# Kernel tuning notes

Hardware: AMD Instinct MI355X
Metric: run time of the kernel (lower is better)

## Reference

```python
import jax, jax.numpy as jnp
import numpy as np

BN_EPS = 1e-5
TN_EPS = 1e-4


def binarize(x):
    # Clipped straight-through binarization (Courbariaux BNN / Brevitas 1-bit):
    # forward = sign(x) in {-1,+1}, backward = hardtanh STE.
    xc = jnp.clip(x, -1.0, 1.0)
    return xc + jax.lax.stop_gradient(jnp.where(x >= 0, 1.0, -1.0).astype(x.dtype) - xc)


def setup_inputs() -> dict:
    key = jax.random.key(0)
    ks = jax.random.split(key, 20)
    B, D, H, C = 16384, 1024, 1024, 10
    inp = {"x": jax.random.uniform(ks[0], (B, D), dtype=jnp.float32)}
    dims = [(H, D), (H, H), (H, H), (C, H)]
    for i, (o, n) in enumerate(dims):
        inp[f"W{i+1}"] = jax.random.uniform(ks[1 + i], (o, n), minval=-1.0, maxval=1.0, dtype=jnp.float32)
    # BatchNorm1d params (eval mode, running stats) for the 3 hidden layers
    for i in range(3):
        k0, k1, k2, k3 = jax.random.split(ks[5 + i], 4)
        inp[f"g{i+1}"] = 1.0 + 0.1 * jax.random.normal(k0, (H,), dtype=jnp.float32)
        inp[f"b{i+1}"] = 0.1 * jax.random.normal(k1, (H,), dtype=jnp.float32)
        inp[f"m{i+1}"] = 0.1 * jax.random.normal(k2, (H,), dtype=jnp.float32)
        inp[f"v{i+1}"] = 0.5 + jax.random.uniform(k3, (H,), dtype=jnp.float32)
    # TensorNorm (scalar norm on the logits)
    inp["tn_w"] = jnp.ones((), dtype=jnp.float32)
    inp["tn_b"] = jnp.zeros((), dtype=jnp.float32)
    inp["tn_m"] = jnp.zeros((), dtype=jnp.float32)
    inp["tn_v"] = jnp.ones((), dtype=jnp.float32)
    return inp


def reference(x, W1, W2, W3, W4,
              g1, b1, m1, v1,
              g2, b2, m2, v2,
              g3, b3, m3, v3,
              tn_w, tn_b, tn_m, tn_v):
    h = binarize(2.0 * x.reshape(x.shape[0], -1) - 1.0)
    # Dropout is identity in eval mode.
    bn = [(g1, b1, m1, v1), (g2, b2, m2, v2), (g3, b3, m3, v3)]
    for W, (g, b, m, v) in zip((W1, W2, W3), bn):
        h = h @ binarize(W).T                      # [B,H] fake-quant linear, no bias
        h = (h - m) * (g * jax.lax.rsqrt(v + BN_EPS)) + b  # BatchNorm1d eval
        h = binarize(h)                            # 1-bit activation quant
    h = h @ binarize(W4).T                         # [B,10]
    # TensorNorm: scalar affine normalization over the whole tensor
    return (h - tn_m) * jax.lax.rsqrt(tn_v + TN_EPS) * tn_w + tn_b
```

## Files before the change

kernel.cpp:

```cpp
#include <hip/hip_runtime.h>
#include <stdint.h>

typedef int  v4i  __attribute__((ext_vector_type(4)));
typedef int  v16i __attribute__((ext_vector_type(16)));
typedef unsigned int uint32;

#define BATCH 16384
#define FEAT  1024

#define OFF_ACTA 0u
#define OFF_ACTB 16777216u
#define OFF_WA1  33554432u
#define OFF_WA2  34603008u
#define OFF_WA3  35651584u
#define OFF_WA4  36700160u
#define OFF_TH   36732928u

__global__ void __launch_bounds__(256) prep_kernel(
    const float* __restrict__ x,
    const float* __restrict__ W1, const float* __restrict__ W2,
    const float* __restrict__ W3, const float* __restrict__ W4,
    const float* __restrict__ g1, const float* __restrict__ b1,
    const float* __restrict__ m1, const float* __restrict__ v1,
    const float* __restrict__ g2, const float* __restrict__ b2,
    const float* __restrict__ m2, const float* __restrict__ v2,
    const float* __restrict__ g3, const float* __restrict__ b3,
    const float* __restrict__ m3, const float* __restrict__ v3,
    char* __restrict__ actA, char* __restrict__ wa1, char* __restrict__ wa2,
    char* __restrict__ wa3, char* __restrict__ wa4, int2* __restrict__ TH)
{
    int b = blockIdx.x;
    if (b == 609) {
        for (int gid = threadIdx.x; gid < 3072; gid += 256) {
            int l = gid >> 10, j = gid & 1023;
            const float *g, *bb, *m, *v;
            if (l == 0)      { g = g1; bb = b1; m = m1; v = v1; }
            else if (l == 1) { g = g2; bb = b2; m = m2; v = v2; }
            else             { g = g3; bb = b3; m = m3; v = v3; }
            double gd = (double)g[j], bd = (double)bb[j], md = (double)m[j], vd = (double)v[j];
            double s = gd / sqrt(vd + 1e-5);
            int ti, flip;
            if (s > 0.0)      { ti = (int)ceil(md - bd / s);  flip = 0; }
            else if (s < 0.0) { ti = (int)floor(md - bd / s); flip = 1; }
            else              { ti = (bd >= 0.0) ? -2000000 : 2000000; flip = 0; }
            TH[gid] = make_int2(ti, flip);
        }
        return;
    }

    const float* src; char* dst; float thr; int nrows; int dblk;
    if (b < 512)      { src = x  + (size_t)b * 32768;            dst = actA; dblk = b;      thr = 0.5f; nrows = 32; }
    else if (b < 544) { int mb = b - 512; src = W1 + (size_t)mb * 32768; dst = wa1; dblk = mb; thr = 0.0f; nrows = 32; }
    else if (b < 576) { int mb = b - 544; src = W2 + (size_t)mb * 32768; dst = wa2; dblk = mb; thr = 0.0f; nrows = 32; }
    else if (b < 608) { int mb = b - 576; src = W3 + (size_t)mb * 32768; dst = wa3; dblk = mb; thr = 0.0f; nrows = 32; }
    else              { src = W4; dst = wa4; dblk = 0; thr = 0.0f; nrows = 10; }

    __shared__ unsigned char T[32][1040];
#pragma unroll
    for (int u = 0; u < 8; ++u) {
        int unit = threadIdx.x + u * 256;
        int row  = unit >> 6;
        int c16  = (unit & 63) << 4;
        uint32 wb0 = 0, wb1 = 0, wb2 = 0, wb3 = 0;
        if (row < nrows) {
            const float* p = src + (size_t)row * 1024 + c16;
            float4 f0 = *(const float4*)(p + 0);
            float4 f1 = *(const float4*)(p + 4);
            float4 f2 = *(const float4*)(p + 8);
            float4 f3 = *(const float4*)(p + 12);
            wb0 = (f0.x>=thr?0x01u:0xFFu) | ((f0.y>=thr?0x01u:0xFFu)<<8) | ((f0.z>=thr?0x01u:0xFFu)<<16) | ((f0.w>=thr?0x01u:0xFFu)<<24);
            wb1 = (f1.x>=thr?0x01u:0xFFu) | ((f1.y>=thr?0x01u:0xFFu)<<8) | ((f1.z>=thr?0x01u:0xFFu)<<16) | ((f1.w>=thr?0x01u:0xFFu)<<24);
            wb2 = (f2.x>=thr?0x01u:0xFFu) | ((f2.y>=thr?0x01u:0xFFu)<<8) | ((f2.z>=thr?0x01u:0xFFu)<<16) | ((f2.w>=thr?0x01u:0xFFu)<<24);
            wb3 = (f3.x>=thr?0x01u:0xFFu) | ((f3.y>=thr?0x01u:0xFFu)<<8) | ((f3.z>=thr?0x01u:0xFFu)<<16) | ((f3.w>=thr?0x01u:0xFFu)<<24);
        }
        *(uint4*)&T[row][c16] = make_uint4(wb0, wb1, wb2, wb3);
    }
    __syncthreads();

    int lane = threadIdx.x & 63;
    int wv   = threadIdx.x >> 6;
    int row  = lane & 31;
    int hb   = (lane >> 5) * 4;
#pragma unroll
    for (int u = 0; u < 8; ++u) {
        int kk = wv * 8 + u;
        const unsigned char* tr = &T[row][kk * 32 + hb];
        uint32 w0 = *(const uint32*)(tr + 0);
        uint32 w1 = *(const uint32*)(tr + 8);
        uint32 w2 = *(const uint32*)(tr + 16);
        uint32 w3 = *(const uint32*)(tr + 24);
        *(uint4*)(dst + (((size_t)dblk * 32 + kk) * 64 + lane) * 16) = make_uint4(w0, w1, w2, w3);
    }
}

__global__ void __launch_bounds__(256, 2) gemm_i8_kernel(
    const v4i* __restrict__ Af, const v4i* __restrict__ Bin,
    const int2* __restrict__ th, v4i* __restrict__ Bout)
{
    __shared__ v4i Bs[2][2048];
    const int tid  = threadIdx.x;
    const int lane = tid & 63;
    const int wv   = tid >> 6;
    int bid = blockIdx.x;
    int xcd = bid & 7;
    int i   = bid >> 3;
    int s   = xcd + ((i >> 3) << 3);
    int m   = i & 7;
    int mt  = m * 4 + wv;
    int nb0 = s * 8;

    v4i r[8];
    {
        const v4i* srcp = Bin + (size_t)nb0 * 2048;
#pragma unroll
        for (int j = 0; j < 8; ++j) r[j] = srcp[j * 256 + tid];
    }
    v4i a[32];
    {
        const v4i* Ap = Af + (size_t)mt * 2048;
#pragma unroll
        for (int kk = 0; kk < 32; ++kk) a[kk] = Ap[kk * 64 + lane];
    }
    int tt[16], tf[16];
    {
        const int2* thp = th + mt * 32;
        int hi4 = (lane >> 5) * 4;
#pragma unroll
        for (int q = 0; q < 16; ++q) {
            int2 t = thp[(q & 3) + 8 * (q >> 2) + hi4];
            tt[q] = t.x; tf[q] = t.y;
        }
    }
#pragma unroll
    for (int j = 0; j < 8; ++j) Bs[0][j * 256 + tid] = r[j];
    __syncthreads();

    int buf = 0;
#pragma unroll 1
    for (int it = 0; it < 8; ++it) {
        if (it < 7) {
            const v4i* srcp = Bin + (size_t)(nb0 + it + 1) * 2048;
#pragma unroll
            for (int j = 0; j < 8; ++j) r[j] = srcp[j * 256 + tid];
        }
        v16i acc;
#pragma unroll
        for (int z = 0; z < 16; ++z) acc[z] = 0;
#pragma unroll
        for (int kk = 0; kk < 32; ++kk) {
            v4i bfrag = Bs[buf][kk * 64 + lane];
            acc = __builtin_amdgcn_mfma_i32_32x32x32_i8(a[kk], bfrag, acc, 0, 0, 0);
        }
        uint32 wds0 = 0, wds1 = 0, wds2 = 0, wds3 = 0;
#pragma unroll
        for (int bq = 0; bq < 4; ++bq) {
            { int q = bq;      int h = acc[q]; int bit = tf[q] ? (h <= tt[q]) : (h >= tt[q]); wds0 |= (bit ? 0x01u : 0xFFu) << (8 * bq); }
            { int q = 4 + bq;  int h = acc[q]; int bit = tf[q] ? (h <= tt[q]) : (h >= tt[q]); wds1 |= (bit ? 0x01u : 0xFFu) << (8 * bq); }
            { int q = 8 + bq;  int h = acc[q]; int bit = tf[q] ? (h <= tt[q]) : (h >= tt[q]); wds2 |= (bit ? 0x01u : 0xFFu) << (8 * bq); }
            { int q = 12 + bq; int h = acc[q]; int bit = tf[q] ? (h <= tt[q]) : (h >= tt[q]); wds3 |= (bit ? 0x01u : 0xFFu) << (8 * bq); }
        }
        v4i ov; ov[0] = (int)wds0; ov[1] = (int)wds1; ov[2] = (int)wds2; ov[3] = (int)wds3;
        Bout[((size_t)(nb0 + it) * 32 + mt) * 64 + lane] = ov;

        if (it < 7) {
#pragma unroll
            for (int j = 0; j < 8; ++j) Bs[buf ^ 1][j * 256 + tid] = r[j];
            __syncthreads();
            buf ^= 1;
        }
    }
}

__global__ void __launch_bounds__(256) final_kernel(
    const v4i* __restrict__ Af4, const v4i* __restrict__ B3,
    const float* __restrict__ tw, const float* __restrict__ tb,
    const float* __restrict__ tm, const float* __restrict__ tv,
    float* __restrict__ out)
{
    int lane = threadIdx.x & 63;
    int nb   = blockIdx.x * 4 + (threadIdx.x >> 6);
    const v4i* Bf = B3 + (size_t)nb * 2048;
    v16i acc;
#pragma unroll
    for (int z = 0; z < 16; ++z) acc[z] = 0;
#pragma unroll
    for (int kk = 0; kk < 32; ++kk) {
        v4i av = Af4[kk * 64 + lane];
        v4i bv = Bf[kk * 64 + lane];
        acc = __builtin_amdgcn_mfma_i32_32x32x32_i8(av, bv, acc, 0, 0, 0);
    }
    double sc  = (double)tw[0] / sqrt((double)tv[0] + 1e-4);
    double off = (double)tb[0] - (double)tm[0] * sc;
    int colg = nb * 32 + (lane & 31);
    int hi   = lane >> 5;
#pragma unroll
    for (int q = 0; q < 8; ++q) {
        int rr = (q & 3) + 8 * (q >> 2) + 4 * hi;
        if (rr < 10)
            out[(size_t)colg * 10 + rr] = (float)((double)acc[q] * sc + off);
    }
}

extern "C" void kernel_launch(void* const* d_in, const int* in_sizes, int n_in,
                              void* d_out, int out_size, void* d_ws, size_t ws_size,
                              hipStream_t stream) {
    const float* x  = (const float*)d_in[0];
    const float* W1 = (const float*)d_in[1];
    const float* W2 = (const float*)d_in[2];
    const float* W3 = (const float*)d_in[3];
    const float* W4 = (const float*)d_in[4];
    const float* g1 = (const float*)d_in[5];
    const float* b1 = (const float*)d_in[6];
    const float* m1 = (const float*)d_in[7];
    const float* v1 = (const float*)d_in[8];
    const float* g2 = (const float*)d_in[9];
    const float* b2 = (const float*)d_in[10];
    const float* m2 = (const float*)d_in[11];
    const float* v2 = (const float*)d_in[12];
    const float* g3 = (const float*)d_in[13];
    const float* b3 = (const float*)d_in[14];
    const float* m3 = (const float*)d_in[15];
    const float* v3 = (const float*)d_in[16];
    const float* tw = (const float*)d_in[17];
    const float* tb = (const float*)d_in[18];
    const float* tm = (const float*)d_in[19];
    const float* tv = (const float*)d_in[20];

    char* ws = (char*)d_ws;
    char* actA = ws + OFF_ACTA;
    char* actB = ws + OFF_ACTB;
    char* wa1  = ws + OFF_WA1;
    char* wa2  = ws + OFF_WA2;
    char* wa3  = ws + OFF_WA3;
    char* wa4  = ws + OFF_WA4;
    int2* TH   = (int2*)(ws + OFF_TH);

    prep_kernel<<<610, 256, 0, stream>>>(x, W1, W2, W3, W4,
                                         g1, b1, m1, v1, g2, b2, m2, v2,
                                         g3, b3, m3, v3,
                                         actA, wa1, wa2, wa3, wa4, TH);

    gemm_i8_kernel<<<512, 256, 0, stream>>>((const v4i*)wa1, (const v4i*)actA, TH,        (v4i*)actB);
    gemm_i8_kernel<<<512, 256, 0, stream>>>((const v4i*)wa2, (const v4i*)actB, TH + 1024, (v4i*)actA);
    gemm_i8_kernel<<<512, 256, 0, stream>>>((const v4i*)wa3, (const v4i*)actA, TH + 2048, (v4i*)actB);

    final_kernel<<<128, 256, 0, stream>>>((const v4i*)wa4, (const v4i*)actB,
                                          tw, tb, tm, tv, (float*)d_out);
}
```

Measured before the change: 206.8 us.

## Stage GEMM B tiles directly into LDS and split MFMA accumulator chain

The GEMM kernel now copies each B tile from global memory straight into shared memory with global_load_lds, instead of loading it into registers and writing it out afterwards. The double-buffer handoff uses explicit vmcnt waits plus a raw s_barrier in place of __syncthreads. The 32-step MFMA chain is also split into two independent accumulators that are summed before thresholding, which shortens the dependency chain. This removes the register staging buffer and the LDS store instructions, but the correctness of the vmcnt(1) wait depends on how loads and the interleaved output store are counted.

Result: faster. 200.1 us (-3.2%).

```diff
diff --git a/kernel.cpp b/kernel.cpp
--- a/kernel.cpp
+++ b/kernel.cpp
@@ -93,6 +93,20 @@
     }
 }
 
+__device__ __forceinline__ void stage_tile(v4i (*Bs)[2048], int bufi,
+                                           const v4i* __restrict__ Bin,
+                                           int tile, int wv, int lane) {
+#pragma unroll
+    for (int j = 0; j < 8; ++j) {
+        __builtin_amdgcn_global_load_lds(
+            (const __attribute__((address_space(1))) void*)
+                (Bin + (size_t)tile * 2048 + j * 256 + wv * 64 + lane),
+            (__attribute__((address_space(3))) void*)
+                (&Bs[bufi][j * 256 + wv * 64]),
+            16, 0, 0);
+    }
+}
+
 __global__ void __launch_bounds__(256, 2) gemm_i8_kernel(
     const v4i* __restrict__ Af, const v4i* __restrict__ Bin,
     const int2* __restrict__ th, v4i* __restrict__ Bout)
@@ -109,12 +123,8 @@
     int mt  = m * 4 + wv;
     int nb0 = s * 8;
 
-    v4i r[8];
-    {
-        const v4i* srcp = Bin + (size_t)nb0 * 2048;
-#pragma unroll
-        for (int j = 0; j < 8; ++j) r[j] = srcp[j * 256 + tid];
-    }
+    stage_tile(Bs, 0, Bin, nb0, wv, lane);
+
     v4i a[32];
     {
         const v4i* Ap = Af + (size_t)mt * 2048;
@@ -131,41 +141,39 @@
             tt[q] = t.x; tf[q] = t.y;
         }
     }
-#pragma unroll
-    for (int j = 0; j < 8; ++j) Bs[0][j * 256 + tid] = r[j];
-    __syncthreads();
+    asm volatile("s_waitcnt vmcnt(0)" ::: "memory");
+    __builtin_amdgcn_s_barrier();
 
     int buf = 0;
 #pragma unroll 1
     for (int it = 0; it < 8; ++it) {
-        if (it < 7) {
-            const v4i* srcp = Bin + (size_t)(nb0 + it + 1) * 2048;
-#pragma unroll
-            for (int j = 0; j < 8; ++j) r[j] = srcp[j * 256 + tid];
-        }
-        v16i acc;
-#pragma unroll
-        for (int z = 0; z < 16; ++z) acc[z] = 0;
-#pragma unroll
-        for (int kk = 0; kk < 32; ++kk) {
-            v4i bfrag = Bs[buf][kk * 64 + lane];
-            acc = __builtin_amdgcn_mfma_i32_32x32x32_i8(a[kk], bfrag, acc, 0, 0, 0);
-        }
+        if (it < 7) stage_tile(Bs, buf ^ 1, Bin, nb0 + it + 1, wv, lane);
+
+        v16i acc0, acc1;
+#pragma unroll
+        for (int z = 0; z < 16; ++z) { acc0[z] = 0; acc1[z] = 0; }
+#pragma unroll
+        for (int kk = 0; kk < 16; ++kk) {
+            v4i b0 = Bs[buf][kk * 64 + lane];
+            v4i b1 = Bs[buf][(kk + 16) * 64 + lane];
+            acc0 = __builtin_amdgcn_mfma_i32_32x32x32_i8(a[kk],      b0, acc0, 0, 0, 0);
+            acc1 = __builtin_amdgcn_mfma_i32_32x32x32_i8(a[kk + 16], b1, acc1, 0, 0, 0);
+        }
+
         uint32 wds0 = 0, wds1 = 0, wds2 = 0, wds3 = 0;
 #pragma unroll
         for (int bq = 0; bq < 4; ++bq) {
-            { int q = bq;      int h = acc[q]; int bit = tf[q] ? (h <= tt[q]) : (h >= tt[q]); wds0 |= (bit ? 0x01u : 0xFFu) << (8 * bq); }
-            { int q = 4 + bq;  int h = acc[q]; int bit = tf[q] ? (h <= tt[q]) : (h >= tt[q]); wds1 |= (bit ? 0x01u : 0xFFu) << (8 * bq); }
-            { int q = 8 + bq;  int h = acc[q]; int bit = tf[q] ? (h <= tt[q]) : (h >= tt[q]); wds2 |= (bit ? 0x01u : 0xFFu) << (8 * bq); }
-            { int q = 12 + bq; int h = acc[q]; int bit = tf[q] ? (h <= tt[q]) : (h >= tt[q]); wds3 |= (bit ? 0x01u : 0xFFu) << (8 * bq); }
+            { int q = bq;      int h = acc0[q] + acc1[q]; int bit = tf[q] ? (h <= tt[q]) : (h >= tt[q]); wds0 |= (bit ? 0x01u : 0xFFu) << (8 * bq); }
+            { int q = 4 + bq;  int h = acc0[q] + acc1[q]; int bit = tf[q] ? (h <= tt[q]) : (h >= tt[q]); wds1 |= (bit ? 0x01u : 0xFFu) << (8 * bq); }
+            { int q = 8 + bq;  int h = acc0[q] + acc1[q]; int bit = tf[q] ? (h <= tt[q]) : (h >= tt[q]); wds2 |= (bit ? 0x01u : 0xFFu) << (8 * bq); }
+            { int q = 12 + bq; int h = acc0[q] + acc1[q]; int bit = tf[q] ? (h <= tt[q]) : (h >= tt[q]); wds3 |= (bit ? 0x01u : 0xFFu) << (8 * bq); }
         }
         v4i ov; ov[0] = (int)wds0; ov[1] = (int)wds1; ov[2] = (int)wds2; ov[3] = (int)wds3;
         Bout[((size_t)(nb0 + it) * 32 + mt) * 64 + lane] = ov;
 
         if (it < 7) {
-#pragma unroll
-            for (int j = 0; j < 8; ++j) Bs[buf ^ 1][j * 256 + tid] = r[j];
-            __syncthreads();
+            asm volatile("s_waitcnt vmcnt(1)" ::: "memory");
+            __builtin_amdgcn_s_barrier();
             buf ^= 1;
         }
     }
```
